# Kernel optimization log

Measured on AMD Instinct MI355X. Metric: run time of the kernel, lower is better.

The kernel has to match this reference:

```python
import jax, jax.numpy as jnp
import numpy as np

N_WAY = 5
NKPTS = 17
EMBED = 512
N_SUPPORT = 25  # 5-way 5-shot
N_QUERY = 65536


def setup_inputs() -> dict:
    key = jax.random.key(0)
    ks = jax.random.split(key, 12)
    def lin(k, fan_in, fan_out):
        return jax.random.normal(k, (fan_in, fan_out), jnp.float32) / np.float32(np.sqrt(fan_in))
    return {
        'support_features': jax.random.normal(ks[0], (1, N_SUPPORT, EMBED), jnp.float32),
        'support_keypoints': jax.random.uniform(ks[1], (N_SUPPORT, NKPTS, 2), jnp.float32),
        'query_features': jax.random.normal(ks[2], (N_QUERY, EMBED), jnp.float32),
        'image_coords': jax.random.uniform(ks[3], (N_QUERY, 2), jnp.float32) * 512.0,
        'W1': lin(ks[4], EMBED, EMBED), 'b1': jnp.zeros((EMBED,), jnp.float32),
        'W2': lin(ks[5], EMBED, EMBED), 'b2': jnp.zeros((EMBED,), jnp.float32),
        'Wo1': lin(ks[6], EMBED, EMBED // 2), 'bo1': jnp.zeros((EMBED // 2,), jnp.float32),
        'Wo2': lin(ks[7], EMBED // 2, 2), 'bo2': jnp.zeros((2,), jnp.float32),
        'Wc1': lin(ks[8], EMBED, EMBED // 2), 'bc1': jnp.zeros((EMBED // 2,), jnp.float32),
        'Wc2': lin(ks[9], EMBED // 2, 1), 'bc2': jnp.zeros((1,), jnp.float32),
        'temperature': jnp.float32(1.0),
    }


def reference(support_features, support_keypoints, query_features, image_coords,
              W1, b1, W2, b2, Wo1, bo1, Wo2, bo2, Wc1, bc1, Wc2, bc2, temperature):
    eps = 1e-8
    nkpts = support_keypoints.shape[1]
    n_query = query_features.shape[0]
    D = query_features.shape[-1]

    # --- compute_prototypes (batch_size == 1; per-kpt prototype identical by construction) ---
    sf = support_features.reshape(-1, D)                      # [Ns, D]
    h = jnp.maximum(sf @ W1 + b1, 0.0) @ W2 + b2              # prototype_net MLP
    n_per = h.shape[0] // N_WAY
    proto_way = h.reshape(N_WAY, n_per, D).mean(axis=1)       # [n_way, D]
    prototypes = jnp.broadcast_to(proto_way[:, None, :], (N_WAY, nkpts, D))

    # --- compute_distances: 1 - cosine_sim, scaled by temperature ---
    qn = jnp.linalg.norm(query_features, axis=-1)             # [Nq]
    pn = jnp.linalg.norm(proto_way, axis=-1)                  # [n_way]
    sim = (query_features @ proto_way.T) / jnp.maximum(qn[:, None] * pn[None, :], eps)
    dist_way = (1.0 - sim) / temperature                      # [Nq, n_way]
    distances = jnp.broadcast_to(dist_way[:, :, None], (n_query, N_WAY, nkpts))

    # --- predict_keypoints ---
    # avg over kpts is a no-op (identical per kpt); argmin over ways
    class_predictions = jnp.argmin(dist_way, axis=1)          # [Nq] int
    # softmax over a single scalar == 1.0, so keypoints == offset broadcast over kpts
    offset = jnp.maximum(query_features @ Wo1 + bo1, 0.0) @ Wo2 + bo2   # [Nq, 2]
    conf = jax.nn.sigmoid(jnp.maximum(query_features @ Wc1 + bc1, 0.0) @ Wc2 + bc2)  # [Nq, 1]
    keypoints = jnp.broadcast_to(offset[:, None, :], (n_query, nkpts, 2))
    keypoints = jax.nn.sigmoid(keypoints) * image_coords[:, None, :]    # image_coords provided
    confidence = jnp.broadcast_to(conf, (n_query, nkpts))

    return keypoints, confidence, distances, class_predictions, prototypes
```

## Files before the change

kernel.cpp:

```cpp
#include <hip/hip_runtime.h>
#include <hip/hip_bf16.h>

#define NQ 65536
#define DIM 512
#define HID 256
#define NWAY 5
#define NKPTS 17

typedef short bf16x8 __attribute__((ext_vector_type(8)));
typedef float f32x4 __attribute__((ext_vector_type(4)));
typedef _Float16 half8 __attribute__((ext_vector_type(8)));

static __device__ __forceinline__ unsigned short f2bf(float f) {
    unsigned int x = __float_as_uint(f);
    unsigned int r = (x + 0x7fffu + ((x >> 16) & 1u)) >> 16;
    return (unsigned short)r;
}

__global__ __launch_bounds__(256) void k_sup1(const float* __restrict__ sf,
                                              const float* __restrict__ W1, const float* __restrict__ b1,
                                              float* __restrict__ ws_h1) {
    int w = blockIdx.x * 4 + (threadIdx.x >> 6);
    int lane = threadIdx.x & 63;
    int s = w >> 9;
    int c = w & 511;
    const float* ip = sf + s * DIM + lane * 8;
    float4 a0 = *(const float4*)ip;
    float4 a1 = *(const float4*)(ip + 4);
    float av[8] = {a0.x, a0.y, a0.z, a0.w, a1.x, a1.y, a1.z, a1.w};
    float acc = 0.0f;
    #pragma unroll
    for (int j = 0; j < 8; j++)
        acc += av[j] * W1[(lane * 8 + j) * DIM + c];
    #pragma unroll
    for (int off = 32; off > 0; off >>= 1)
        acc += __shfl_xor(acc, off, 64);
    if (lane == 0)
        ws_h1[s * DIM + c] = fmaxf(acc + b1[c], 0.0f);
}

__global__ __launch_bounds__(256) void k_mid(const float* __restrict__ ws_h1,
                                             const float* __restrict__ W2, const float* __restrict__ b2,
                                             const float* __restrict__ Wo1, const float* __restrict__ Wc1,
                                             float* __restrict__ ws_proto, unsigned short* __restrict__ wb) {
    int bx = blockIdx.x;
    int t = threadIdx.x;
    if (bx < 640) {
        int g = bx * 4 + (t >> 6);
        int lane = t & 63;
        int w = g >> 9;
        int c = g & 511;
        const float* base = ws_h1 + (w * 5) * DIM + lane * 8;
        float av[8] = {0, 0, 0, 0, 0, 0, 0, 0};
        #pragma unroll
        for (int s = 0; s < 5; s++) {
            float4 x0 = *(const float4*)(base + s * DIM);
            float4 x1 = *(const float4*)(base + s * DIM + 4);
            av[0] += x0.x; av[1] += x0.y; av[2] += x0.z; av[3] += x0.w;
            av[4] += x1.x; av[5] += x1.y; av[6] += x1.z; av[7] += x1.w;
        }
        float acc = 0.0f;
        #pragma unroll
        for (int j = 0; j < 8; j++)
            acc += (av[j] * 0.2f) * W2[(lane * 8 + j) * DIM + c];
        #pragma unroll
        for (int off = 32; off > 0; off >>= 1)
            acc += __shfl_xor(acc, off, 64);
        if (lane == 0)
            ws_proto[w * DIM + c] = acc + b2[c];
    } else {
        __shared__ unsigned short T[64][72];
        int tb = bx - 640;
        const float* src = (tb < 32) ? Wo1 : Wc1;
        int cofs = (tb < 32) ? 0 : 256;
        int tt = tb & 31;
        int kt = tt >> 2;
        int ct = tt & 3;
        int i = t >> 2;
        int qd = t & 3;
        const float* rp = src + (size_t)(kt * 64 + i) * HID + ct * 64 + qd * 16;
        #pragma unroll
        for (int v = 0; v < 4; v++) {
            float4 x = *(const float4*)(rp + v * 4);
            T[qd * 16 + v * 4 + 0][i] = f2bf(x.x);
            T[qd * 16 + v * 4 + 1][i] = f2bf(x.y);
            T[qd * 16 + v * 4 + 2][i] = f2bf(x.z);
            T[qd * 16 + v * 4 + 3][i] = f2bf(x.w);
        }
        __syncthreads();
        int j = t >> 2;
        int part = t & 3;
        uint4 o0 = *(const uint4*)&T[j][part * 16];
        uint4 o1 = *(const uint4*)&T[j][part * 16 + 8];
        unsigned short* dst = wb + (size_t)(cofs + ct * 64 + j) * DIM + kt * 64 + part * 16;
        *(uint4*)dst = o0;
        *(uint4*)(dst + 8) = o1;
    }
}

__global__ __launch_bounds__(256) void k_fused(const float* __restrict__ qf, const unsigned short* __restrict__ wb,
                                               const float* __restrict__ ws_proto,
                                               const float* __restrict__ temp_p,
                                               const float* __restrict__ bo1, const float* __restrict__ Wo2,
                                               const float* __restrict__ bo2,
                                               const float* __restrict__ bc1, const float* __restrict__ Wc2,
                                               const float* __restrict__ bc2,
                                               const float* __restrict__ ic,
                                               float* __restrict__ out_kp, float* __restrict__ out_conf,
                                               float* __restrict__ out_dist, float* __restrict__ out_class,
                                               float* __restrict__ out_proto) {
    __shared__ __align__(16) char smem[37376];
    unsigned short* Alds = (unsigned short*)smem;
    unsigned short* Blds = (unsigned short*)(smem + 5120);
    float* s_proto = (float*)(smem + 25600);
    float* dlds = (float*)(smem + 35840);
    float* pn_lds = (float*)(smem + 37120);
    _Float16* hlds = (_Float16*)smem;
    float* offlds = (float*)(smem + 33792);

    int bx = blockIdx.x;
    int mb = bx >> 1;
    int nb = bx & 1;
    int t = threadIdx.x;
    int wv = t >> 6;
    int lane = t & 63;
    int r = lane & 15;
    int q8 = (lane >> 4) * 8;

    if (bx < 85 && t < 128) {
        f32x4 v = *(const f32x4*)(ws_proto + (bx / NKPTS) * DIM + t * 4);
        *(f32x4*)(out_proto + (size_t)bx * DIM + t * 4) = v;
    }

    f32x4 acc[4][4];
    #pragma unroll
    for (int i = 0; i < 4; i++)
        #pragma unroll
        for (int j = 0; j < 4; j++) {
            f32x4 z = {0.0f, 0.0f, 0.0f, 0.0f};
            acc[i][j] = z;
        }

    int am = t >> 2;
    int akc = t & 3;
    int mine = ((t >> 7) == nb);
    const float* aptr = qf + ((size_t)(mb * 64 + am)) * DIM + akc * 8;
    const unsigned short* bptr = wb + ((size_t)(nb * 256 + t)) * DIM;

    for (int i = t; i < NWAY * DIM; i += 256) s_proto[i] = ws_proto[i];

    float ds[NWAY] = {0, 0, 0, 0, 0};
    float qq = 0.0f;

    float4 A0 = *(const float4*)(aptr);
    float4 A1 = *(const float4*)(aptr + 4);
    uint4 B0 = *(const uint4*)(bptr);
    uint4 B1 = *(const uint4*)(bptr + 8);
    uint4 B2 = *(const uint4*)(bptr + 16);
    uint4 B3 = *(const uint4*)(bptr + 24);

    for (int it = 0; it < 16; it++) {
        unsigned int p0 = f2bf(A0.x) | ((unsigned int)f2bf(A0.y) << 16);
        unsigned int p1 = f2bf(A0.z) | ((unsigned int)f2bf(A0.w) << 16);
        unsigned int p2 = f2bf(A1.x) | ((unsigned int)f2bf(A1.y) << 16);
        unsigned int p3 = f2bf(A1.z) | ((unsigned int)f2bf(A1.w) << 16);
        float av[8] = {A0.x, A0.y, A0.z, A0.w, A1.x, A1.y, A1.z, A1.w};
        __syncthreads();
        *(uint4*)(Alds + am * 40 + akc * 8) = make_uint4(p0, p1, p2, p3);
        *(uint4*)(Blds + t * 40) = B0;
        *(uint4*)(Blds + t * 40 + 8) = B1;
        *(uint4*)(Blds + t * 40 + 16) = B2;
        *(uint4*)(Blds + t * 40 + 24) = B3;
        __syncthreads();
        if (it < 15) {
            int k1 = (it + 1) * 32;
            A0 = *(const float4*)(aptr + k1);
            A1 = *(const float4*)(aptr + k1 + 4);
            B0 = *(const uint4*)(bptr + k1);
            B1 = *(const uint4*)(bptr + k1 + 8);
            B2 = *(const uint4*)(bptr + k1 + 16);
            B3 = *(const uint4*)(bptr + k1 + 24);
        }
        if (mine) {
            int kb = it * 32 + akc * 8;
            #pragma unroll
            for (int w = 0; w < NWAY; w++) {
                f32x4 pv0 = *(const f32x4*)(s_proto + w * DIM + kb);
                f32x4 pv1 = *(const f32x4*)(s_proto + w * DIM + kb + 4);
                ds[w] += av[0] * pv0[0] + av[1] * pv0[1] + av[2] * pv0[2] + av[3] * pv0[3]
                       + av[4] * pv1[0] + av[5] * pv1[1] + av[6] * pv1[2] + av[7] * pv1[3];
            }
            #pragma unroll
            for (int j = 0; j < 8; j++) qq += av[j] * av[j];
        }
        bf16x8 af[4], bf[4];
        #pragma unroll
        for (int mt = 0; mt < 4; mt++)
            af[mt] = *(const bf16x8*)(Alds + (mt * 16 + r) * 40 + q8);
        #pragma unroll
        for (int nt = 0; nt < 4; nt++)
            bf[nt] = *(const bf16x8*)(Blds + (wv * 64 + nt * 16 + r) * 40 + q8);
        #pragma unroll
        for (int mt = 0; mt < 4; mt++)
            #pragma unroll
            for (int nt = 0; nt < 4; nt++)
                acc[mt][nt] = __builtin_amdgcn_mfma_f32_16x16x32_bf16(af[mt], bf[nt], acc[mt][nt], 0, 0, 0);
    }

    for (int w = wv; w < NWAY; w += 4) {
        f32x4 a = *(const f32x4*)(s_proto + w * DIM + lane * 8);
        f32x4 b = *(const f32x4*)(s_proto + w * DIM + lane * 8 + 4);
        float ss = a[0]*a[0] + a[1]*a[1] + a[2]*a[2] + a[3]*a[3]
                 + b[0]*b[0] + b[1]*b[1] + b[2]*b[2] + b[3]*b[3];
        #pragma unroll
        for (int off = 32; off > 0; off >>= 1) ss += __shfl_xor(ss, off, 64);
        if (lane == 0) pn_lds[w] = sqrtf(ss);
    }
    if (mine) {
        #pragma unroll
        for (int off = 1; off <= 2; off <<= 1) {
            #pragma unroll
            for (int w = 0; w < NWAY; w++) ds[w] += __shfl_xor(ds[w], off, 64);
            qq += __shfl_xor(qq, off, 64);
        }
    }
    __syncthreads();
    if (mine && akc == 0) {
        float qn = sqrtf(qq);
        float invt = 1.0f / temp_p[0];
        float mv = 1e30f;
        int ami = 0;
        #pragma unroll
        for (int w = 0; w < NWAY; w++) {
            float den = fmaxf(qn * pn_lds[w], 1e-8f);
            float d = (1.0f - ds[w] / den) * invt;
            dlds[am * 5 + w] = d;
            if (d < mv) { mv = d; ami = w; }
        }
        out_class[mb * 64 + am] = (float)ami;
    }
    __syncthreads();

    {
        int qlo = nb * 32;
        for (int i = t; i < 32 * NWAY * NKPTS; i += 256) {
            int q = qlo + i / (NWAY * NKPTS);
            int rem = i - (i / (NWAY * NKPTS)) * (NWAY * NKPTS);
            out_dist[(size_t)(mb * 64 + q) * (NWAY * NKPTS) + rem] = dlds[q * 5 + rem / NKPTS];
        }
    }

    const float* bias = nb ? bc1 : bo1;
    #pragma unroll
    for (int nt = 0; nt < 4; nt++) {
        int cl = wv * 64 + nt * 16 + r;
        float bv = bias[cl];
        #pragma unroll
        for (int mt = 0; mt < 4; mt++)
            #pragma unroll
            for (int rg = 0; rg < 4; rg++) {
                int ml = mt * 16 + (lane >> 4) * 4 + rg;
                float v = acc[mt][nt][rg] + bv;
                hlds[ml * 264 + cl] = (_Float16)fmaxf(v, 0.0f);
            }
    }
    __syncthreads();

    if (nb == 0) {
        if (t < 64) {
            float ox = bo2[0], oy = bo2[1];
            for (int c0 = 0; c0 < 256; c0 += 8) {
                half8 hv = *(const half8*)(hlds + t * 264 + c0);
                #pragma unroll
                for (int j = 0; j < 8; j++) {
                    float hf = (float)hv[j];
                    ox += hf * Wo2[(c0 + j) * 2];
                    oy += hf * Wo2[(c0 + j) * 2 + 1];
                }
            }
            offlds[t * 2] = ox;
            offlds[t * 2 + 1] = oy;
        }
        __syncthreads();
        for (int i = t; i < 64 * 34; i += 256) {
            int q = i / 34;
            int rem = i - q * 34;
            int j = rem & 1;
            size_t Q = (size_t)mb * 64 + q;
            float o = offlds[q * 2 + j];
            float sg = 1.0f / (1.0f + __expf(-o));
            out_kp[Q * 34 + rem] = sg * ic[Q * 2 + j];
        }
    } else {
        if (t < 64) {
            float cl2 = bc2[0];
            for (int c0 = 0; c0 < 256; c0 += 8) {
                half8 hv = *(const half8*)(hlds + t * 264 + c0);
                #pragma unroll
                for (int j = 0; j < 8; j++) cl2 += (float)hv[j] * Wc2[c0 + j];
            }
            offlds[t] = 1.0f / (1.0f + __expf(-cl2));
        }
        __syncthreads();
        for (int i = t; i < 64 * 17; i += 256) {
            int q = i / 17;
            out_conf[(size_t)mb * 64 * 17 + i] = offlds[q];
        }
    }
}

extern "C" void kernel_launch(void* const* d_in, const int* in_sizes, int n_in,
                              void* d_out, int out_size, void* d_ws, size_t ws_size,
                              hipStream_t stream) {
    const float* sf = (const float*)d_in[0];
    const float* qf = (const float*)d_in[2];
    const float* ic = (const float*)d_in[3];
    const float* W1 = (const float*)d_in[4];
    const float* b1 = (const float*)d_in[5];
    const float* W2 = (const float*)d_in[6];
    const float* b2 = (const float*)d_in[7];
    const float* Wo1 = (const float*)d_in[8];
    const float* bo1 = (const float*)d_in[9];
    const float* Wo2 = (const float*)d_in[10];
    const float* bo2 = (const float*)d_in[11];
    const float* Wc1 = (const float*)d_in[12];
    const float* bc1 = (const float*)d_in[13];
    const float* Wc2 = (const float*)d_in[14];
    const float* bc2 = (const float*)d_in[15];
    const float* temp = (const float*)d_in[16];

    float* out = (float*)d_out;
    float* out_kp = out;
    float* out_conf = out + 2228224;
    float* out_dist = out + 3342336;
    float* out_class = out + 8912896;
    float* out_proto = out + 8978432;

    char* ws = (char*)d_ws;
    float* ws_h1 = (float*)ws;
    float* ws_proto = (float*)(ws + 51200);
    unsigned short* ws_wb = (unsigned short*)(ws + 65536);

    hipLaunchKernelGGL(k_sup1, dim3(3200), dim3(256), 0, stream, sf, W1, b1, ws_h1);
    hipLaunchKernelGGL(k_mid, dim3(704), dim3(256), 0, stream, ws_h1, W2, b2, Wo1, Wc1, ws_proto, ws_wb);
    hipLaunchKernelGGL(k_fused, dim3(2048), dim3(256), 0, stream, qf, ws_wb, ws_proto, temp,
                       bo1, Wo2, bo2, bc1, Wc2, bc2, ic, out_kp, out_conf, out_dist, out_class, out_proto);
}
```

Baseline: 366.1 us.

## Split distance and GEMM kernels, widen GEMM tile to full 512 columns

Restructures the pipeline: the support MLP becomes two small kernels (layer 1 fused with the weight transpose, layer 2 also computing the prototype norms). Cosine distances and argmin move into their own kernel that reads the query rows separately. The GEMM kernel now covers all 512 output columns per 64-row block, so each query tile is loaded and converted once instead of twice. The second-layer dot products are reduced directly from registers with shuffles instead of through an fp16 LDS staging buffer. The cost is a second full read of the query features and an extra launch, plus heavier register and LDS use in the GEMM, which may lower occupancy.

```diff
diff --git a/kernel.cpp b/kernel.cpp
--- a/kernel.cpp
+++ b/kernel.cpp
@@ -9,7 +9,6 @@
 
 typedef short bf16x8 __attribute__((ext_vector_type(8)));
 typedef float f32x4 __attribute__((ext_vector_type(4)));
-typedef _Float16 half8 __attribute__((ext_vector_type(8)));
 
 static __device__ __forceinline__ unsigned short f2bf(float f) {
     unsigned int x = __float_as_uint(f);
@@ -17,60 +16,24 @@
     return (unsigned short)r;
 }
 
-__global__ __launch_bounds__(256) void k_sup1(const float* __restrict__ sf,
-                                              const float* __restrict__ W1, const float* __restrict__ b1,
-                                              float* __restrict__ ws_h1) {
-    int w = blockIdx.x * 4 + (threadIdx.x >> 6);
-    int lane = threadIdx.x & 63;
-    int s = w >> 9;
-    int c = w & 511;
-    const float* ip = sf + s * DIM + lane * 8;
-    float4 a0 = *(const float4*)ip;
-    float4 a1 = *(const float4*)(ip + 4);
-    float av[8] = {a0.x, a0.y, a0.z, a0.w, a1.x, a1.y, a1.z, a1.w};
-    float acc = 0.0f;
-    #pragma unroll
-    for (int j = 0; j < 8; j++)
-        acc += av[j] * W1[(lane * 8 + j) * DIM + c];
-    #pragma unroll
-    for (int off = 32; off > 0; off >>= 1)
-        acc += __shfl_xor(acc, off, 64);
-    if (lane == 0)
+__global__ __launch_bounds__(256) void k_l1(const float* __restrict__ sf,
+                                            const float* __restrict__ W1, const float* __restrict__ b1,
+                                            const float* __restrict__ Wo1, const float* __restrict__ Wc1,
+                                            float* __restrict__ ws_h1, unsigned short* __restrict__ wb) {
+    int bx = blockIdx.x, t = threadIdx.x;
+    if (bx < 50) {
+        __shared__ float s_sf[DIM];
+        int s = bx >> 1, c = (bx & 1) * 256 + t;
+        s_sf[t] = sf[s * DIM + t];
+        s_sf[t + 256] = sf[s * DIM + 256 + t];
+        __syncthreads();
+        float acc = 0.0f;
+        #pragma unroll 8
+        for (int k = 0; k < DIM; k++) acc += W1[k * DIM + c] * s_sf[k];
         ws_h1[s * DIM + c] = fmaxf(acc + b1[c], 0.0f);
-}
-
-__global__ __launch_bounds__(256) void k_mid(const float* __restrict__ ws_h1,
-                                             const float* __restrict__ W2, const float* __restrict__ b2,
-                                             const float* __restrict__ Wo1, const float* __restrict__ Wc1,
-                                             float* __restrict__ ws_proto, unsigned short* __restrict__ wb) {
-    int bx = blockIdx.x;
-    int t = threadIdx.x;
-    if (bx < 640) {
-        int g = bx * 4 + (t >> 6);
-        int lane = t & 63;
-        int w = g >> 9;
-        int c = g & 511;
-        const float* base = ws_h1 + (w * 5) * DIM + lane * 8;
-        float av[8] = {0, 0, 0, 0, 0, 0, 0, 0};
-        #pragma unroll
-        for (int s = 0; s < 5; s++) {
-            float4 x0 = *(const float4*)(base + s * DIM);
-            float4 x1 = *(const float4*)(base + s * DIM + 4);
-            av[0] += x0.x; av[1] += x0.y; av[2] += x0.z; av[3] += x0.w;
-            av[4] += x1.x; av[5] += x1.y; av[6] += x1.z; av[7] += x1.w;
-        }
-        float acc = 0.0f;
-        #pragma unroll
-        for (int j = 0; j < 8; j++)
-            acc += (av[j] * 0.2f) * W2[(lane * 8 + j) * DIM + c];
-        #pragma unroll
-        for (int off = 32; off > 0; off >>= 1)
-            acc += __shfl_xor(acc, off, 64);
-        if (lane == 0)
-            ws_proto[w * DIM + c] = acc + b2[c];
     } else {
         __shared__ unsigned short T[64][72];
-        int tb = bx - 640;
+        int tb = bx - 50;
         const float* src = (tb < 32) ? Wo1 : Wc1;
         int cofs = (tb < 32) ? 0 : 256;
         int tt = tb & 31;
@@ -98,215 +61,244 @@
     }
 }
 
-__global__ __launch_bounds__(256) void k_fused(const float* __restrict__ qf, const unsigned short* __restrict__ wb,
-                                               const float* __restrict__ ws_proto,
-                                               const float* __restrict__ temp_p,
-                                               const float* __restrict__ bo1, const float* __restrict__ Wo2,
-                                               const float* __restrict__ bo2,
-                                               const float* __restrict__ bc1, const float* __restrict__ Wc2,
-                                               const float* __restrict__ bc2,
-                                               const float* __restrict__ ic,
-                                               float* __restrict__ out_kp, float* __restrict__ out_conf,
-                                               float* __restrict__ out_dist, float* __restrict__ out_class,
-                                               float* __restrict__ out_proto) {
-    __shared__ __align__(16) char smem[37376];
-    unsigned short* Alds = (unsigned short*)smem;
-    unsigned short* Blds = (unsigned short*)(smem + 5120);
-    float* s_proto = (float*)(smem + 25600);
-    float* dlds = (float*)(smem + 35840);
-    float* pn_lds = (float*)(smem + 37120);
-    _Float16* hlds = (_Float16*)smem;
-    float* offlds = (float*)(smem + 33792);
-
-    int bx = blockIdx.x;
-    int mb = bx >> 1;
-    int nb = bx & 1;
+__global__ __launch_bounds__(256) void k_l2(const float* __restrict__ ws_h1,
+                                            const float* __restrict__ W2, const float* __restrict__ b2,
+                                            float* __restrict__ ws_proto, float* __restrict__ ws_pn) {
+    __shared__ float s_m[DIM];
+    __shared__ float red[256];
+    int w = blockIdx.x, t = threadIdx.x;
+    for (int k = t; k < DIM; k += 256) {
+        float m = 0.0f;
+        #pragma unroll
+        for (int s = 0; s < 5; s++) m += ws_h1[(w * 5 + s) * DIM + k];
+        s_m[k] = m * 0.2f;
+    }
+    __syncthreads();
+    float a0 = 0.0f, a1 = 0.0f;
+    int c0 = t, c1 = t + 256;
+    #pragma unroll 8
+    for (int k = 0; k < DIM; k++) {
+        float mk = s_m[k];
+        a0 += W2[k * DIM + c0] * mk;
+        a1 += W2[k * DIM + c1] * mk;
+    }
+    float v0 = a0 + b2[c0], v1 = a1 + b2[c1];
+    ws_proto[w * DIM + c0] = v0;
+    ws_proto[w * DIM + c1] = v1;
+    red[t] = v0 * v0 + v1 * v1;
+    __syncthreads();
+    for (int s2 = 128; s2 > 0; s2 >>= 1) {
+        if (t < s2) red[t] += red[t + s2];
+        __syncthreads();
+    }
+    if (t == 0) ws_pn[w] = sqrtf(red[0]);
+}
+
+__global__ __launch_bounds__(256) void k_cd(const float* __restrict__ qf,
+                                            const float* __restrict__ ws_proto, const float* __restrict__ ws_pn,
+                                            const float* __restrict__ temp_p,
+                                            float* __restrict__ out_dist, float* __restrict__ out_class,
+                                            float* __restrict__ out_proto) {
+    __shared__ float dl[32][5];
+    __shared__ float cl[32];
+    int bx = blockIdx.x, t = threadIdx.x;
+    int wv = t >> 6, lane = t & 63;
+
+    if (bx < NWAY * NKPTS && t < 128) {
+        f32x4 v = *(const f32x4*)(ws_proto + (bx / NKPTS) * DIM + t * 4);
+        *(f32x4*)(out_proto + (size_t)bx * DIM + t * 4) = v;
+    }
+
+    float p[NWAY][8];
+    #pragma unroll
+    for (int w = 0; w < NWAY; w++) {
+        f32x4 u0 = *(const f32x4*)(ws_proto + w * DIM + lane * 8);
+        f32x4 u1 = *(const f32x4*)(ws_proto + w * DIM + lane * 8 + 4);
+        p[w][0] = u0[0]; p[w][1] = u0[1]; p[w][2] = u0[2]; p[w][3] = u0[3];
+        p[w][4] = u1[0]; p[w][5] = u1[1]; p[w][6] = u1[2]; p[w][7] = u1[3];
+    }
+    float pn[NWAY];
+    #pragma unroll
+    for (int w = 0; w < NWAY; w++) pn[w] = ws_pn[w];
+    float invt = 1.0f / temp_p[0];
+
+    for (int i = 0; i < 8; i++) {
+        int rloc = wv * 8 + i;
+        size_t rq = (size_t)bx * 32 + rloc;
+        const float4* qp = (const float4*)(qf + rq * DIM + lane * 8);
+        float4 a = qp[0], b = qp[1];
+        float qv[8] = {a.x, a.y, a.z, a.w, b.x, b.y, b.z, b.w};
+        float s[6] = {0, 0, 0, 0, 0, 0};
+        #pragma unroll
+        for (int j = 0; j < 8; j++) {
+            float v = qv[j];
+            s[5] += v * v;
+            #pragma unroll
+            for (int w = 0; w < NWAY; w++) s[w] += v * p[w][j];
+        }
+        #pragma unroll
+        for (int off = 32; off > 0; off >>= 1)
+            #pragma unroll
+            for (int k = 0; k < 6; k++) s[k] += __shfl_xor(s[k], off, 64);
+        if (lane == 0) {
+            float qn = sqrtf(s[5]);
+            float mv = 1e30f;
+            int ami = 0;
+            #pragma unroll
+            for (int w = 0; w < NWAY; w++) {
+                float den = fmaxf(qn * pn[w], 1e-8f);
+                float d = (1.0f - s[w] / den) * invt;
+                dl[rloc][w] = d;
+                if (d < mv) { mv = d; ami = w; }
+            }
+            cl[rloc] = (float)ami;
+        }
+    }
+    __syncthreads();
+    for (int i = t; i < 32 * NWAY * NKPTS; i += 256) {
+        int q = i / (NWAY * NKPTS);
+        int rem = i - q * (NWAY * NKPTS);
+        out_dist[(size_t)bx * 32 * (NWAY * NKPTS) + i] = dl[q][rem / NKPTS];
+    }
+    if (t < 32) out_class[(size_t)bx * 32 + t] = cl[t];
+}
+
+__global__ __launch_bounds__(256) void k_gemm(const float* __restrict__ qf, const unsigned short* __restrict__ wb,
+                                              const float* __restrict__ bo1, const float* __restrict__ Wo2,
+                                              const float* __restrict__ bo2,
+                                              const float* __restrict__ bc1, const float* __restrict__ Wc2,
+                                              const float* __restrict__ bc2,
+                                              const float* __restrict__ ic,
+                                              float* __restrict__ out_kp, float* __restrict__ out_conf) {
+    __shared__ __align__(16) unsigned short Alds[64 * 40];
+    __shared__ __align__(16) unsigned short Blds[512 * 40];
+    __shared__ float exo[2][64], eyo[2][64], ecf[2][64];
+    __shared__ float fin[3][64];
+
+    int mb = blockIdx.x;
     int t = threadIdx.x;
     int wv = t >> 6;
     int lane = t & 63;
     int r = lane & 15;
     int q8 = (lane >> 4) * 8;
 
-    if (bx < 85 && t < 128) {
-        f32x4 v = *(const f32x4*)(ws_proto + (bx / NKPTS) * DIM + t * 4);
-        *(f32x4*)(out_proto + (size_t)bx * DIM + t * 4) = v;
-    }
-
-    f32x4 acc[4][4];
+    f32x4 acc[4][8];
     #pragma unroll
     for (int i = 0; i < 4; i++)
         #pragma unroll
-        for (int j = 0; j < 4; j++) {
+        for (int j = 0; j < 8; j++) {
             f32x4 z = {0.0f, 0.0f, 0.0f, 0.0f};
             acc[i][j] = z;
         }
 
     int am = t >> 2;
     int akc = t & 3;
-    int mine = ((t >> 7) == nb);
     const float* aptr = qf + ((size_t)(mb * 64 + am)) * DIM + akc * 8;
-    const unsigned short* bptr = wb + ((size_t)(nb * 256 + t)) * DIM;
-
-    for (int i = t; i < NWAY * DIM; i += 256) s_proto[i] = ws_proto[i];
-
-    float ds[NWAY] = {0, 0, 0, 0, 0};
-    float qq = 0.0f;
+    const unsigned short* bptr[8];
+    int bldsoff[8];
+    #pragma unroll
+    for (int j = 0; j < 8; j++) {
+        int chunk = j * 256 + t;
+        int col = chunk >> 2, kc = chunk & 3;
+        bptr[j] = wb + (size_t)col * DIM + kc * 8;
+        bldsoff[j] = col * 40 + kc * 8;
+    }
 
     float4 A0 = *(const float4*)(aptr);
     float4 A1 = *(const float4*)(aptr + 4);
-    uint4 B0 = *(const uint4*)(bptr);
-    uint4 B1 = *(const uint4*)(bptr + 8);
-    uint4 B2 = *(const uint4*)(bptr + 16);
-    uint4 B3 = *(const uint4*)(bptr + 24);
+    uint4 Bp[8];
+    #pragma unroll
+    for (int j = 0; j < 8; j++) Bp[j] = *(const uint4*)(bptr[j]);
 
     for (int it = 0; it < 16; it++) {
         unsigned int p0 = f2bf(A0.x) | ((unsigned int)f2bf(A0.y) << 16);
         unsigned int p1 = f2bf(A0.z) | ((unsigned int)f2bf(A0.w) << 16);
         unsigned int p2 = f2bf(A1.x) | ((unsigned int)f2bf(A1.y) << 16);
         unsigned int p3 = f2bf(A1.z) | ((unsigned int)f2bf(A1.w) << 16);
-        float av[8] = {A0.x, A0.y, A0.z, A0.w, A1.x, A1.y, A1.z, A1.w};
         __syncthreads();
         *(uint4*)(Alds + am * 40 + akc * 8) = make_uint4(p0, p1, p2, p3);
-        *(uint4*)(Blds + t * 40) = B0;
-        *(uint4*)(Blds + t * 40 + 8) = B1;
-        *(uint4*)(Blds + t * 40 + 16) = B2;
-        *(uint4*)(Blds + t * 40 + 24) = B3;
+        #pragma unroll
+        for (int j = 0; j < 8; j++) *(uint4*)(Blds + bldsoff[j]) = Bp[j];
         __syncthreads();
         if (it < 15) {
             int k1 = (it + 1) * 32;
             A0 = *(const float4*)(aptr + k1);
             A1 = *(const float4*)(aptr + k1 + 4);
-            B0 = *(const uint4*)(bptr + k1);
-            B1 = *(const uint4*)(bptr + k1 + 8);
-            B2 = *(const uint4*)(bptr + k1 + 16);
-            B3 = *(const uint4*)(bptr + k1 + 24);
-        }
-        if (mine) {
-            int kb = it * 32 + akc * 8;
-            #pragma unroll
-            for (int w = 0; w < NWAY; w++) {
-                f32x4 pv0 = *(const f32x4*)(s_proto + w * DIM + kb);
-                f32x4 pv1 = *(const f32x4*)(s_proto + w * DIM + kb + 4);
-                ds[w] += av[0] * pv0[0] + av[1] * pv0[1] + av[2] * pv0[2] + av[3] * pv0[3]
-                       + av[4] * pv1[0] + av[5] * pv1[1] + av[6] * pv1[2] + av[7] * pv1[3];
-            }
-            #pragma unroll
-            for (int j = 0; j < 8; j++) qq += av[j] * av[j];
-        }
-        bf16x8 af[4], bf[4];
+            #pragma unroll
+            for (int j = 0; j < 8; j++) Bp[j] = *(const uint4*)(bptr[j] + k1);
+        }
+        bf16x8 af[4], bf[8];
         #pragma unroll
         for (int mt = 0; mt < 4; mt++)
             af[mt] = *(const bf16x8*)(Alds + (mt * 16 + r) * 40 + q8);
         #pragma unroll
-        for (int nt = 0; nt < 4; nt++)
-            bf[nt] = *(const bf16x8*)(Blds + (wv * 64 + nt * 16 + r) * 40 + q8);
+        for (int nt = 0; nt < 8; nt++)
+            bf[nt] = *(const bf16x8*)(Blds + (wv * 128 + nt * 16 + r) * 40 + q8);
         #pragma unroll
         for (int mt = 0; mt < 4; mt++)
             #pragma unroll
-            for (int nt = 0; nt < 4; nt++)
+            for (int nt = 0; nt < 8; nt++)
                 acc[mt][nt] = __builtin_amdgcn_mfma_f32_16x16x32_bf16(af[mt], bf[nt], acc[mt][nt], 0, 0, 0);
     }
 
-    for (int w = wv; w < NWAY; w += 4) {
-        f32x4 a = *(const f32x4*)(s_proto + w * DIM + lane * 8);
-        f32x4 b = *(const f32x4*)(s_proto + w * DIM + lane * 8 + 4);
-        float ss = a[0]*a[0] + a[1]*a[1] + a[2]*a[2] + a[3]*a[3]
-                 + b[0]*b[0] + b[1]*b[1] + b[2]*b[2] + b[3]*b[3];
-        #pragma unroll
-        for (int off = 32; off > 0; off >>= 1) ss += __shfl_xor(ss, off, 64);
-        if (lane == 0) pn_lds[w] = sqrtf(ss);
-    }
-    if (mine) {
-        #pragma unroll
-        for (int off = 1; off <= 2; off <<= 1) {
-            #pragma unroll
-            for (int w = 0; w < NWAY; w++) ds[w] += __shfl_xor(ds[w], off, 64);
-            qq += __shfl_xor(qq, off, 64);
-        }
-    }
-    __syncthreads();
-    if (mine && akc == 0) {
-        float qn = sqrtf(qq);
-        float invt = 1.0f / temp_p[0];
-        float mv = 1e30f;
-        int ami = 0;
-        #pragma unroll
-        for (int w = 0; w < NWAY; w++) {
-            float den = fmaxf(qn * pn_lds[w], 1e-8f);
-            float d = (1.0f - ds[w] / den) * invt;
-            dlds[am * 5 + w] = d;
-            if (d < mv) { mv = d; ami = w; }
-        }
-        out_class[mb * 64 + am] = (float)ami;
-    }
-    __syncthreads();
-
-    {
-        int qlo = nb * 32;
-        for (int i = t; i < 32 * NWAY * NKPTS; i += 256) {
-            int q = qlo + i / (NWAY * NKPTS);
-            int rem = i - (i / (NWAY * NKPTS)) * (NWAY * NKPTS);
-            out_dist[(size_t)(mb * 64 + q) * (NWAY * NKPTS) + rem] = dlds[q * 5 + rem / NKPTS];
-        }
-    }
-
-    const float* bias = nb ? bc1 : bo1;
-    #pragma unroll
-    for (int nt = 0; nt < 4; nt++) {
-        int cl = wv * 64 + nt * 16 + r;
-        float bv = bias[cl];
-        #pragma unroll
-        for (int mt = 0; mt < 4; mt++)
-            #pragma unroll
-            for (int rg = 0; rg < 4; rg++) {
-                int ml = mt * 16 + (lane >> 4) * 4 + rg;
-                float v = acc[mt][nt][rg] + bv;
-                hlds[ml * 264 + cl] = (_Float16)fmaxf(v, 0.0f);
+    float bv[8], wx[8], wy[8];
+    if (wv < 2) {
+        #pragma unroll
+        for (int nt = 0; nt < 8; nt++) {
+            int col = wv * 128 + nt * 16 + r;
+            bv[nt] = bo1[col];
+            wx[nt] = Wo2[col * 2];
+            wy[nt] = Wo2[col * 2 + 1];
+        }
+    } else {
+        #pragma unroll
+        for (int nt = 0; nt < 8; nt++) {
+            int cc = (wv - 2) * 128 + nt * 16 + r;
+            bv[nt] = bc1[cc];
+            wx[nt] = Wc2[cc];
+            wy[nt] = 0.0f;
+        }
+    }
+    #pragma unroll
+    for (int mt = 0; mt < 4; mt++)
+        #pragma unroll
+        for (int rg = 0; rg < 4; rg++) {
+            float hx = 0.0f, hy = 0.0f;
+            #pragma unroll
+            for (int nt = 0; nt < 8; nt++) {
+                float h = fmaxf(acc[mt][nt][rg] + bv[nt], 0.0f);
+                hx += h * wx[nt];
+                hy += h * wy[nt];
             }
-    }
-    __syncthreads();
-
-    if (nb == 0) {
-        if (t < 64) {
-            float ox = bo2[0], oy = bo2[1];
-            for (int c0 = 0; c0 < 256; c0 += 8) {
-                half8 hv = *(const half8*)(hlds + t * 264 + c0);
-                #pragma unroll
-                for (int j = 0; j < 8; j++) {
-                    float hf = (float)hv[j];
-                    ox += hf * Wo2[(c0 + j) * 2];
-                    oy += hf * Wo2[(c0 + j) * 2 + 1];
-                }
+            #pragma unroll
+            for (int off = 1; off <= 8; off <<= 1) {
+                hx += __shfl_xor(hx, off, 64);
+                hy += __shfl_xor(hy, off, 64);
             }
-            offlds[t * 2] = ox;
-            offlds[t * 2 + 1] = oy;
-        }
-        __syncthreads();
-        for (int i = t; i < 64 * 34; i += 256) {
-            int q = i / 34;
-            int rem = i - q * 34;
-            int j = rem & 1;
-            size_t Q = (size_t)mb * 64 + q;
-            float o = offlds[q * 2 + j];
-            float sg = 1.0f / (1.0f + __expf(-o));
-            out_kp[Q * 34 + rem] = sg * ic[Q * 2 + j];
-        }
-    } else {
-        if (t < 64) {
-            float cl2 = bc2[0];
-            for (int c0 = 0; c0 < 256; c0 += 8) {
-                half8 hv = *(const half8*)(hlds + t * 264 + c0);
-                #pragma unroll
-                for (int j = 0; j < 8; j++) cl2 += (float)hv[j] * Wc2[c0 + j];
+            if (r == 0) {
+                int row = mt * 16 + (lane >> 4) * 4 + rg;
+                if (wv < 2) { exo[wv][row] = hx; eyo[wv][row] = hy; }
+                else        { ecf[wv - 2][row] = hx; }
             }
-            offlds[t] = 1.0f / (1.0f + __expf(-cl2));
-        }
-        __syncthreads();
-        for (int i = t; i < 64 * 17; i += 256) {
-            int q = i / 17;
-            out_conf[(size_t)mb * 64 * 17 + i] = offlds[q];
-        }
-    }
+        }
+    __syncthreads();
+    if (t < 64) {
+        size_t Q = (size_t)mb * 64 + t;
+        float ox = exo[0][t] + exo[1][t] + bo2[0];
+        float oy = eyo[0][t] + eyo[1][t] + bo2[1];
+        float cf = ecf[0][t] + ecf[1][t] + bc2[0];
+        fin[0][t] = (1.0f / (1.0f + __expf(-ox))) * ic[Q * 2];
+        fin[1][t] = (1.0f / (1.0f + __expf(-oy))) * ic[Q * 2 + 1];
+        fin[2][t] = 1.0f / (1.0f + __expf(-cf));
+    }
+    __syncthreads();
+    for (int i = t; i < 64 * 34; i += 256) {
+        int q = i / 34;
+        int rem = i - q * 34;
+        out_kp[(size_t)mb * 64 * 34 + i] = fin[rem & 1][q];
+    }
+    for (int i = t; i < 64 * 17; i += 256)
+        out_conf[(size_t)mb * 64 * 17 + i] = fin[2][i / 17];
 }
 
 extern "C" void kernel_launch(void* const* d_in, const int* in_sizes, int n_in,
@@ -339,10 +331,13 @@
     char* ws = (char*)d_ws;
     float* ws_h1 = (float*)ws;
     float* ws_proto = (float*)(ws + 51200);
+    float* ws_pn = (float*)(ws + 61440);
     unsigned short* ws_wb = (unsigned short*)(ws + 65536);
 
-    hipLaunchKernelGGL(k_sup1, dim3(3200), dim3(256), 0, stream, sf, W1, b1, ws_h1);
-    hipLaunchKernelGGL(k_mid, dim3(704), dim3(256), 0, stream, ws_h1, W2, b2, Wo1, Wc1, ws_proto, ws_wb);
-    hipLaunchKernelGGL(k_fused, dim3(2048), dim3(256), 0, stream, qf, ws_wb, ws_proto, temp,
-                       bo1, Wo2, bo2, bc1, Wc2, bc2, ic, out_kp, out_conf, out_dist, out_class, out_proto);
-}
+    hipLaunchKernelGGL(k_l1, dim3(114), dim3(256), 0, stream, sf, W1, b1, Wo1, Wc1, ws_h1, ws_wb);
+    hipLaunchKernelGGL(k_l2, dim3(5), dim3(256), 0, stream, ws_h1, W2, b2, ws_proto, ws_pn);
+    hipLaunchKernelGGL(k_cd, dim3(2048), dim3(256), 0, stream, qf, ws_proto, ws_pn, temp,
+                       out_dist, out_class, out_proto);
+    hipLaunchKernelGGL(k_gemm, dim3(1024), dim3(256), 0, stream, qf, ws_wb,
+                       bo1, Wo2, bo2, bc1, Wc2, bc2, ic, out_kp, out_conf);
+}
```

Measured after the change: 501.7 us. +37.0%, slower.
